# Kernel tuning notes

Hardware: AMD Instinct MI355X
Metric: run time of the kernel (lower is better)

Reference implementation:

```python
import jax, jax.numpy as jnp
import numpy as np

N_HEAD, D_MODEL, D_K, D_V = 8, 512, 64, 64
WINDOW, THRESH = 2, 0.5
TEMP = float(np.sqrt(D_K))
LN_EPS = 1e-5


def setup_inputs() -> dict:
    key = jax.random.key(0)
    ks = jax.random.split(key, 12)
    B, L = 4, 2048
    std_qk = np.sqrt(2.0 / (D_MODEL + D_K))
    std_v = np.sqrt(2.0 / (D_MODEL + D_V))
    return {
        "q": jax.random.normal(ks[0], (B, L, D_MODEL), jnp.float32),
        "k": jax.random.normal(ks[1], (B, L, D_MODEL), jnp.float32),
        "v": jax.random.normal(ks[2], (B, L, D_MODEL), jnp.float32),
        "w_q": jax.random.normal(ks[3], (N_HEAD * D_K, D_MODEL), jnp.float32) * std_qk,
        "b_q": jnp.zeros((N_HEAD * D_K,), jnp.float32),
        "w_k": jax.random.normal(ks[4], (N_HEAD * D_K, D_MODEL), jnp.float32) * std_qk,
        "b_k": jnp.zeros((N_HEAD * D_K,), jnp.float32),
        "w_v": jax.random.normal(ks[5], (N_HEAD * D_V, D_MODEL), jnp.float32) * std_v,
        "b_v": jnp.zeros((N_HEAD * D_V,), jnp.float32),
        "w_g": jax.random.normal(ks[6], (1, D_K), jnp.float32) * (1.0 / np.sqrt(D_K)),
        "b_g": jnp.zeros((1,), jnp.float32),
        "w_fc": jax.random.normal(ks[7], (D_MODEL, N_HEAD * D_V), jnp.float32) * (1.0 / np.sqrt(D_MODEL)),
        "b_fc": jnp.zeros((D_MODEL,), jnp.float32),
        "ln_g": jnp.ones((D_MODEL,), jnp.float32),
        "ln_b": jnp.zeros((D_MODEL,), jnp.float32),
    }


def reference(q, k, v, w_q, b_q, w_k, b_k, w_v, b_v, w_g, b_g, w_fc, b_fc, ln_g, ln_b):
    B, Lq, _ = q.shape
    Lk = k.shape[1]
    residual = q
    # project and split heads: (h, B, L, d)
    qh = (q @ w_q.T + b_q).reshape(B, Lq, N_HEAD, D_K).transpose(2, 0, 1, 3)
    kh = (k @ w_k.T + b_k).reshape(B, Lk, N_HEAD, D_K).transpose(2, 0, 1, 3)
    vh = (v @ w_v.T + b_v).reshape(B, Lk, N_HEAD, D_V).transpose(2, 0, 1, 3)

    scores = jnp.einsum('hbqd,hbkd->hbqk', qh, kh) / TEMP  # (h, B, Lq, Lk)

    # dynamic gate: tokens with sigmoid(gate) > THRESH keep full attention,
    # others are restricted to a +/-WINDOW sliding window
    gate_open = jax.nn.sigmoid(jnp.einsum('hbqd,od->hbqo', qh, w_g) + b_g)[..., 0] > THRESH
    i = jnp.arange(Lq)[:, None]
    j = jnp.arange(Lk)[None, :]
    win = jnp.abs(i - j) <= WINDOW  # (Lq, Lk)
    allowed = gate_open[..., None] | win  # (h, B, Lq, Lk)
    scores = jnp.where(allowed, scores, -jnp.inf)

    attn = jax.nn.softmax(scores, axis=-1)  # dropout is identity in eval
    out = jnp.einsum('hbqk,hbkd->hbqd', attn, vh)
    out = out.transpose(1, 2, 0, 3).reshape(B, Lq, N_HEAD * D_V)
    out = out @ w_fc.T + b_fc

    x = out + residual
    mu = jnp.mean(x, axis=-1, keepdims=True)
    var = jnp.mean((x - mu) ** 2, axis=-1, keepdims=True)
    out = (x - mu) * jax.lax.rsqrt(var + LN_EPS) * ln_g + ln_b

    return out, attn.reshape(N_HEAD * B, Lq, Lk)
```

## Files before the change

kernel.cpp:

```cpp
#include <hip/hip_runtime.h>


typedef _Float16 f16;
typedef _Float16 f16x8 __attribute__((ext_vector_type(8)));
typedef _Float16 f16x4 __attribute__((ext_vector_type(4)));
typedef float f32x4 __attribute__((ext_vector_type(4)));

#define OUT0_ELEMS (4 * 2048 * 512)

__device__ __forceinline__ f16x8 cvt8(float4 a, float4 b) {
  f16x8 r;
  r[0] = (f16)a.x; r[1] = (f16)a.y; r[2] = (f16)a.z; r[3] = (f16)a.w;
  r[4] = (f16)b.x; r[5] = (f16)b.y; r[6] = (f16)b.z; r[7] = (f16)b.w;
  return r;
}

__global__ __launch_bounds__(256) void prep_kernel(
    const float* __restrict__ w_q, const float* __restrict__ b_q,
    const float* __restrict__ w_g, const float* __restrict__ b_g,
    double* __restrict__ wge, double* __restrict__ bqg) {
  int idx = blockIdx.x * 256 + threadIdx.x;
  if (idx < 4096) {
    int h = idx >> 9, c = idx & 511;
    double acc = 0.0;
    for (int d = 0; d < 64; ++d)
      acc += (double)w_g[d] * (double)w_q[(h * 64 + d) * 512 + c];
    wge[idx] = acc;
  }
  if (idx < 8) {
    double acc = (double)b_g[0];
    for (int d = 0; d < 64; ++d)
      acc += (double)b_q[idx * 64 + d] * (double)w_g[d];
    bqg[idx] = acc;
  }
}

__global__ __launch_bounds__(256) void gate_kernel(
    const float* __restrict__ q, const double* __restrict__ wge,
    const double* __restrict__ bqg, int* __restrict__ gate) {
  int lane = threadIdx.x & 63, wid = threadIdx.x >> 6;
  int tok = blockIdx.x * 4 + wid;
  int b = tok >> 11, l = tok & 2047;
  const float* qr = q + (long)tok * 512;
  float qv[8];
#pragma unroll
  for (int j = 0; j < 8; ++j) qv[j] = qr[lane + 64 * j];
#pragma unroll
  for (int h = 0; h < 8; ++h) {
    double acc = 0.0;
#pragma unroll
    for (int j = 0; j < 8; ++j) acc += (double)qv[j] * wge[h * 512 + lane + 64 * j];
#pragma unroll
    for (int off = 1; off < 64; off <<= 1) acc += __shfl_xor(acc, off);
    double logit = acc + bqg[h];
    if (lane == 0) gate[(h * 4 + b) * 2048 + l] = (logit > 0.0) ? 1 : 0;
  }
}

template <int EPI>
__global__ __launch_bounds__(256) void gemm512(
    const float* __restrict__ A, const float* __restrict__ W,
    const float* __restrict__ bias, const float* __restrict__ res,
    f16* __restrict__ out16, float* __restrict__ outf) {
  __shared__ __align__(16) f16 As[64 * 32];
  __shared__ __align__(16) f16 Ws[64 * 32];
  const int tid = threadIdx.x;
  const int lane = tid & 63, wid = tid >> 6;
  const int lo = lane & 15, hi = lane >> 4;
  const int m0 = blockIdx.x * 64, n0 = blockIdx.y * 64;
  const int wm = wid >> 1, wn = wid & 1;

  const int srow = tid >> 2, sseg = tid & 3;
  const int ssu = sseg ^ (srow & 3);
  const float* gA = A + (long)(m0 + srow) * 512 + sseg * 8;
  const float* gW = W + (long)(n0 + srow) * 512 + sseg * 8;
  f16* wA = &As[srow * 32 + ssu * 8];
  f16* wW = &Ws[srow * 32 + ssu * 8];

  const f32x4 zero4 = {0.f, 0.f, 0.f, 0.f};
  f32x4 acc[2][2] = {{zero4, zero4}, {zero4, zero4}};
  const int ra0 = wm * 32 + lo;
  const int rb0 = wn * 32 + lo;
  const int sa = hi ^ (ra0 & 3);
  const int sb = hi ^ (rb0 & 3);

  for (int kk = 0; kk < 512; kk += 32) {
    float4 a0 = *(const float4*)(gA + kk);
    float4 a1 = *(const float4*)(gA + kk + 4);
    float4 w0 = *(const float4*)(gW + kk);
    float4 w1 = *(const float4*)(gW + kk + 4);
    *(f16x8*)wA = cvt8(a0, a1);
    *(f16x8*)wW = cvt8(w0, w1);
    __syncthreads();
    f16x8 af0 = *(const f16x8*)&As[ra0 * 32 + sa * 8];
    f16x8 af1 = *(const f16x8*)&As[(ra0 + 16) * 32 + sa * 8];
    f16x8 bf0 = *(const f16x8*)&Ws[rb0 * 32 + sb * 8];
    f16x8 bf1 = *(const f16x8*)&Ws[(rb0 + 16) * 32 + sb * 8];
    acc[0][0] = __builtin_amdgcn_mfma_f32_16x16x32_f16(af0, bf0, acc[0][0], 0, 0, 0);
    acc[0][1] = __builtin_amdgcn_mfma_f32_16x16x32_f16(af0, bf1, acc[0][1], 0, 0, 0);
    acc[1][0] = __builtin_amdgcn_mfma_f32_16x16x32_f16(af1, bf0, acc[1][0], 0, 0, 0);
    acc[1][1] = __builtin_amdgcn_mfma_f32_16x16x32_f16(af1, bf1, acc[1][1], 0, 0, 0);
    __syncthreads();
  }

#pragma unroll
  for (int i = 0; i < 2; ++i)
#pragma unroll
    for (int j = 0; j < 2; ++j)
#pragma unroll
      for (int r = 0; r < 4; ++r) {
        const int m = m0 + wm * 32 + i * 16 + hi * 4 + r;
        const int n = n0 + wn * 32 + j * 16 + lo;
        float v = acc[i][j][r] + bias[n];
        if constexpr (EPI == 0) {
          const int b = m >> 11, l = m & 2047, h = n >> 6, d = n & 63;
          out16[(long)((h * 4 + b) * 2048 + l) * 64 + d] = (f16)v;
        } else if constexpr (EPI == 2) {
          const int b = m >> 11, l = m & 2047, h = n >> 6, d = n & 63;
          out16[(long)((h * 4 + b) * 64 + d) * 2048 + l] = (f16)v;
        } else {
          outf[(long)m * 512 + n] = v + res[(long)m * 512 + n];
        }
      }
}

struct Stg2 { uint4 d0, d1; };

__device__ __forceinline__ Stg2 ldK(const f16* __restrict__ g, int tid) {
  Stg2 s;
  s.d0 = *(const uint4*)(g + tid * 8);
  s.d1 = *(const uint4*)(g + 2048 + tid * 8);
  return s;
}

__device__ __forceinline__ Stg2 ldV(const f16* __restrict__ g, int tid) {
  const int row = tid >> 3, seg = tid & 7;
  const f16* p = g + (long)row * 2048 + seg * 8;
  Stg2 s;
  s.d0 = *(const uint4*)p;
  s.d1 = *(const uint4*)(p + 32 * 2048);
  return s;
}

__device__ __forceinline__ void stW(const Stg2& s, f16* lds, int tid) {
  const int row = tid >> 3, seg = tid & 7, sw = row & 7;
  *(uint4*)&lds[(row << 6) + ((seg ^ sw) << 3)] = s.d0;
  *(uint4*)&lds[((row + 32) << 6) + ((seg ^ sw) << 3)] = s.d1;
}

__global__ __launch_bounds__(256) void attn_kernel(
    const f16* __restrict__ qh, const f16* __restrict__ kh,
    const f16* __restrict__ vt, const int* __restrict__ gate,
    float* __restrict__ attn, float* __restrict__ o) {
  __shared__ __align__(16) f16 Ks[2][4096];
  __shared__ __align__(16) f16 Vs[2][4096];
  __shared__ __align__(16) f16 Ps[4][1024];
  const int tid = threadIdx.x;
  const int lane = tid & 63, wid = tid >> 6;
  const int lo = lane & 15, hi = lane >> 4;
  const int bid = blockIdx.x;
  const int xcd = bid & 7, local = bid >> 3;
  const int hb = xcd * 4 + (local >> 5);
  const int q0 = (local & 31) << 6;

  const f16* khb = kh + (long)hb * 2048 * 64;
  const f16* vtb = vt + (long)hb * 64 * 2048;

  const f16* qrow = qh + (long)(hb * 2048 + q0 + (wid << 4) + lo) * 64;
  const f16x8 aq0 = *(const f16x8*)(qrow + (hi << 3));
  const f16x8 aq1 = *(const f16x8*)(qrow + 32 + (hi << 3));

  int qi[4], gt[4];
  float psum[4];
#pragma unroll
  for (int r = 0; r < 4; ++r) {
    qi[r] = q0 + (wid << 4) + (hi << 2) + r;
    gt[r] = gate[hb * 2048 + qi[r]];
    psum[r] = 0.f;
  }
  const f32x4 zero4 = {0.f, 0.f, 0.f, 0.f};

  {
    Stg2 kreg = ldK(khb, tid);
    stW(kreg, &Ks[0][0], tid);
    kreg = ldK(khb + 4096, tid);
    int cur = 0;
    for (int kt = 0; kt < 32; ++kt) {
      __syncthreads();
      if (kt < 31) {
        stW(kreg, &Ks[cur ^ 1][0], tid);
        if (kt < 30) kreg = ldK(khb + (long)(kt + 2) * 4096, tid);
      }
      const f16* Kc = &Ks[cur][0];
      f32x4 sacc[4] = {zero4, zero4, zero4, zero4};
      __builtin_amdgcn_s_setprio(1);
#pragma unroll
      for (int s = 0; s < 2; ++s) {
        const f16x8 a = s ? aq1 : aq0;
#pragma unroll
        for (int nt = 0; nt < 4; ++nt) {
          const int krow = (nt << 4) + lo;
          const f16x8 b = *(const f16x8*)&Kc[(krow << 6) + ((((s << 2) + hi) ^ (krow & 7)) << 3)];
          sacc[nt] = __builtin_amdgcn_mfma_f32_16x16x32_f16(a, b, sacc[nt], 0, 0, 0);
        }
      }
      __builtin_amdgcn_s_setprio(0);
      const int kkb = (kt << 6) + lo;
#pragma unroll
      for (int nt = 0; nt < 4; ++nt) {
        const int kk = kkb + (nt << 4);
#pragma unroll
        for (int r = 0; r < 4; ++r) {
          const bool allowed = gt[r] || ((unsigned)(kk - qi[r] + 2) <= 4u);
          psum[r] += allowed ? __expf(sacc[nt][r] * 0.125f) : 0.f;
        }
      }
      cur ^= 1;
    }
  }

  float invl[4];
#pragma unroll
  for (int r = 0; r < 4; ++r) {
    float s = psum[r];
    s += __shfl_xor(s, 1);
    s += __shfl_xor(s, 2);
    s += __shfl_xor(s, 4);
    s += __shfl_xor(s, 8);
    invl[r] = 1.f / s;
  }

  f32x4 oacc[4] = {zero4, zero4, zero4, zero4};
  f16* Pw = &Ps[wid][0];
  const int row2 = lane >> 2, qq = lane & 3;
  float* arow = attn + (long)(hb * 2048 + q0 + (wid << 4) + row2) * 2048;

  {
    Stg2 kreg = ldK(khb, tid);
    Stg2 vreg = ldV(vtb, tid);
    stW(kreg, &Ks[0][0], tid);
    stW(vreg, &Vs[0][0], tid);
    kreg = ldK(khb + 4096, tid);
    vreg = ldV(vtb + 64, tid);
    int cur = 0;
    for (int kt = 0; kt < 32; ++kt) {
      __syncthreads();
      if (kt < 31) {
        stW(kreg, &Ks[cur ^ 1][0], tid);
        stW(vreg, &Vs[cur ^ 1][0], tid);
        if (kt < 30) {
          kreg = ldK(khb + (long)(kt + 2) * 4096, tid);
          vreg = ldV(vtb + ((kt + 2) << 6), tid);
        }
      }
      const f16* Kc = &Ks[cur][0];
      const f16* Vc = &Vs[cur][0];
      f32x4 sacc[4] = {zero4, zero4, zero4, zero4};
      __builtin_amdgcn_s_setprio(1);
#pragma unroll
      for (int s = 0; s < 2; ++s) {
        const f16x8 a = s ? aq1 : aq0;
#pragma unroll
        for (int nt = 0; nt < 4; ++nt) {
          const int krow = (nt << 4) + lo;
          const f16x8 b = *(const f16x8*)&Kc[(krow << 6) + ((((s << 2) + hi) ^ (krow & 7)) << 3)];
          sacc[nt] = __builtin_amdgcn_mfma_f32_16x16x32_f16(a, b, sacc[nt], 0, 0, 0);
        }
      }
      __builtin_amdgcn_s_setprio(0);
      const int kkb = (kt << 6) + lo;
#pragma unroll
      for (int nt = 0; nt < 4; ++nt) {
        const int kk = kkb + (nt << 4);
#pragma unroll
        for (int r = 0; r < 4; ++r) {
          const bool allowed = gt[r] || ((unsigned)(kk - qi[r] + 2) <= 4u);
          const float p = allowed ? __expf(sacc[nt][r] * 0.125f) * invl[r] : 0.f;
          const int prow = (hi << 2) + r;
          const int pcol = (nt << 4) + lo;
          Pw[(prow << 6) + (((pcol >> 3) ^ (prow & 7)) << 3) + (pcol & 7)] = (f16)p;
        }
      }
      __builtin_amdgcn_s_setprio(1);
#pragma unroll
      for (int s = 0; s < 2; ++s) {
        const f16x8 ap = *(const f16x8*)&Pw[(lo << 6) + ((((s << 2) + hi) ^ (lo & 7)) << 3)];
#pragma unroll
        for (int nt = 0; nt < 4; ++nt) {
          const int vrow = (nt << 4) + lo;
          const f16x8 bv = *(const f16x8*)&Vc[(vrow << 6) + ((((s << 2) + hi) ^ (vrow & 7)) << 3)];
          oacc[nt] = __builtin_amdgcn_mfma_f32_16x16x32_f16(ap, bv, oacc[nt], 0, 0, 0);
        }
      }
      __builtin_amdgcn_s_setprio(0);
      {
        const int swz = row2 & 7;
        float* dst = arow + (kt << 6) + (qq << 2);
#pragma unroll
        for (int i = 0; i < 4; ++i) {
          const f16x4 pv = *(const f16x4*)&Pw[(row2 << 6) + ((((i << 1) + (qq >> 1)) ^ swz) << 3) + ((qq & 1) << 2)];
          f32x4 fo = {(float)pv[0], (float)pv[1], (float)pv[2], (float)pv[3]};
          *(f32x4*)(dst + (i << 4)) = fo;
        }
      }
      cur ^= 1;
    }
  }

  const int b = hb & 3, h = hb >> 2;
#pragma unroll
  for (int nt = 0; nt < 4; ++nt)
#pragma unroll
    for (int r = 0; r < 4; ++r)
      o[(long)(b * 2048 + qi[r]) * 512 + (h << 6) + (nt << 4) + lo] = oacc[nt][r];
}

__global__ __launch_bounds__(256) void ln_kernel(float* __restrict__ x,
                                                 const float* __restrict__ g,
                                                 const float* __restrict__ bta) {
  __shared__ float red[8];
  const int t = threadIdx.x;
  float* row = x + (long)blockIdx.x * 512;
  float v0 = row[t], v1 = row[t + 256];
  float s = v0 + v1;
#pragma unroll
  for (int off = 1; off < 64; off <<= 1) s += __shfl_xor(s, off);
  if ((t & 63) == 0) red[t >> 6] = s;
  __syncthreads();
  const float mean = (red[0] + red[1] + red[2] + red[3]) * (1.f / 512.f);
  const float d0 = v0 - mean, d1 = v1 - mean;
  float sq = d0 * d0 + d1 * d1;
#pragma unroll
  for (int off = 1; off < 64; off <<= 1) sq += __shfl_xor(sq, off);
  if ((t & 63) == 0) red[4 + (t >> 6)] = sq;
  __syncthreads();
  const float var = (red[4] + red[5] + red[6] + red[7]) * (1.f / 512.f);
  const float rstd = 1.f / sqrtf(var + 1e-5f);
  row[t] = d0 * rstd * g[t] + bta[t];
  row[t + 256] = d1 * rstd * g[t + 256] + bta[t + 256];
}

extern "C" void kernel_launch(void* const* d_in, const int* in_sizes, int n_in,
                              void* d_out, int out_size, void* d_ws, size_t ws_size,
                              hipStream_t stream) {
  const float* q    = (const float*)d_in[0];
  const float* k    = (const float*)d_in[1];
  const float* v    = (const float*)d_in[2];
  const float* w_q  = (const float*)d_in[3];
  const float* b_q  = (const float*)d_in[4];
  const float* w_k  = (const float*)d_in[5];
  const float* b_k  = (const float*)d_in[6];
  const float* w_v  = (const float*)d_in[7];
  const float* b_v  = (const float*)d_in[8];
  const float* w_g  = (const float*)d_in[9];
  const float* b_g  = (const float*)d_in[10];
  const float* w_fc = (const float*)d_in[11];
  const float* b_fc = (const float*)d_in[12];
  const float* ln_g = (const float*)d_in[13];
  const float* ln_b = (const float*)d_in[14];

  char* wsb = (char*)d_ws;
  f16* qh16   = (f16*)wsb;
  f16* kh16   = qh16 + 4194304;
  f16* vt16   = kh16 + 4194304;
  float* ob   = (float*)(wsb + 25165824);
  int* gateb  = (int*)(wsb + 25165824 + 16777216);
  double* wge = (double*)(wsb + 25165824 + 16777216 + 262144);
  double* bqg = wge + 4096;

  float* out0 = (float*)d_out;
  float* attn = out0 + OUT0_ELEMS;

  prep_kernel<<<16, 256, 0, stream>>>(w_q, b_q, w_g, b_g, wge, bqg);
  gate_kernel<<<2048, 256, 0, stream>>>(q, wge, bqg, gateb);

  dim3 gp(128, 8);
  gemm512<0><<<gp, 256, 0, stream>>>(q, w_q, b_q, nullptr, qh16, nullptr);
  gemm512<0><<<gp, 256, 0, stream>>>(k, w_k, b_k, nullptr, kh16, nullptr);
  gemm512<2><<<gp, 256, 0, stream>>>(v, w_v, b_v, nullptr, vt16, nullptr);

  attn_kernel<<<1024, 256, 0, stream>>>(qh16, kh16, vt16, gateb, attn, ob);

  gemm512<3><<<gp, 256, 0, stream>>>(ob, w_fc, b_fc, q, nullptr, out0);
  ln_kernel<<<8192, 256, 0, stream>>>(out0, ln_g, ln_b);
}
```

Before: 299.4 us.

## Compact gated query rows and handle closed rows with a windowed fast path

Adds a per-head-batch compaction kernel that partitions query rows into gate-open and gate-closed lists. Full dense attention blocks now run only over open rows, addressed through the permutation, and exit early past the open count. Closed rows go to extra blocks that zero the attention row and compute only the 5-wide window softmax and PV product directly. This removes the full QK and PV work for closed rows, at the cost of an extra launch, scattered row addressing, and a serial per-row path for closed rows.

```diff
diff --git a/kernel.cpp b/kernel.cpp
--- a/kernel.cpp
+++ b/kernel.cpp
@@ -55,6 +55,39 @@
     double logit = acc + bqg[h];
     if (lane == 0) gate[(h * 4 + b) * 2048 + l] = (logit > 0.0) ? 1 : 0;
   }
+}
+
+__global__ __launch_bounds__(256) void compact_kernel(
+    const int* __restrict__ gate, unsigned short* __restrict__ perm,
+    int* __restrict__ nopen) {
+  __shared__ int wsum[4];
+  const int hb = blockIdx.x, t = threadIdx.x;
+  const int lane = t & 63, wid = t >> 6;
+  const int base = hb * 2048;
+  int g[8];
+  int cnt = 0;
+#pragma unroll
+  for (int i = 0; i < 8; ++i) { g[i] = gate[base + t * 8 + i]; cnt += g[i]; }
+  int inc = cnt;
+#pragma unroll
+  for (int off = 1; off < 64; off <<= 1) {
+    int y = __shfl_up(inc, off);
+    if (lane >= off) inc += y;
+  }
+  if (lane == 63) wsum[wid] = inc;
+  __syncthreads();
+  int wbase = 0;
+  for (int w = 0; w < wid; ++w) wbase += wsum[w];
+  const int totOpen = wsum[0] + wsum[1] + wsum[2] + wsum[3];
+  int openPos = wbase + inc - cnt;
+  int closedPos = totOpen + t * 8 - openPos;
+#pragma unroll
+  for (int i = 0; i < 8; ++i) {
+    int l = t * 8 + i;
+    if (g[i]) perm[base + openPos++] = (unsigned short)l;
+    else      perm[base + closedPos++] = (unsigned short)l;
+  }
+  if (t == 0) nopen[hb] = totOpen;
 }
 
 template <int EPI>
@@ -151,22 +184,91 @@
 __global__ __launch_bounds__(256) void attn_kernel(
     const f16* __restrict__ qh, const f16* __restrict__ kh,
     const f16* __restrict__ vt, const int* __restrict__ gate,
+    const unsigned short* __restrict__ perm, const int* __restrict__ nopen,
     float* __restrict__ attn, float* __restrict__ o) {
   __shared__ __align__(16) f16 Ks[2][4096];
   __shared__ __align__(16) f16 Vs[2][4096];
   __shared__ __align__(16) f16 Ps[4][1024];
   const int tid = threadIdx.x;
   const int lane = tid & 63, wid = tid >> 6;
+  const int bid = blockIdx.x;
+
+  if (bid >= 1024) {
+    const int vb = bid - 1024;
+    const int hb = vb >> 5, chunk = vb & 31;
+    const int nop = nopen[hb];
+    const int j0 = ((nop + 63) & ~63) + (chunk << 6);
+    if (j0 >= 2048) return;
+    unsigned short* rowIdx = (unsigned short*)&Ks[0][0];
+    if (tid < 64) rowIdx[tid] = perm[hb * 2048 + j0 + tid];
+    __syncthreads();
+    float* abase = attn + ((long)hb * 2048 << 11);
+    const f32x4 zero4 = {0.f, 0.f, 0.f, 0.f};
+#pragma unroll 4
+    for (int it = 0; it < 128; ++it) {
+      const int c = tid + (it << 8);
+      const int ri = c >> 9;
+      const int col = (c & 511) << 2;
+      *(f32x4*)(abase + ((long)rowIdx[ri] << 11) + col) = zero4;
+    }
+    __syncthreads();
+    const f16* qhb = qh + (long)hb * 2048 * 64;
+    const f16* khb = kh + (long)hb * 2048 * 64;
+    const f16* vtb = vt + (long)hb * 64 * 2048;
+    const int b = hb & 3, h = hb >> 2;
+    for (int rr = 0; rr < 16; ++rr) {
+      const int row = rowIdx[(wid << 4) + rr];
+      const int jlo = max(row - 2, 0), jhi = min(row + 2, 2047);
+      const float qv = (float)qhb[(long)row * 64 + lane];
+      float p0, p1, p2, p3, p4, sum = 0.f;
+#pragma unroll
+      for (int jj = 0; jj < 5; ++jj) {
+        const int j = jlo + jj;
+        const int js = min(j, 2047);
+        float prod = qv * (float)khb[(long)js * 64 + lane];
+        prod += __shfl_xor(prod, 1);
+        prod += __shfl_xor(prod, 2);
+        prod += __shfl_xor(prod, 4);
+        prod += __shfl_xor(prod, 8);
+        prod += __shfl_xor(prod, 16);
+        prod += __shfl_xor(prod, 32);
+        const float e = (j <= jhi) ? __expf(prod * 0.125f) : 0.f;
+        if (jj == 0) p0 = e; else if (jj == 1) p1 = e; else if (jj == 2) p2 = e;
+        else if (jj == 3) p3 = e; else p4 = e;
+        sum += e;
+      }
+      const float inv = 1.f / sum;
+      float pv = p0;
+      pv = (lane == 1) ? p1 : pv;
+      pv = (lane == 2) ? p2 : pv;
+      pv = (lane == 3) ? p3 : pv;
+      pv = (lane == 4) ? p4 : pv;
+      if (lane < 5 && (jlo + lane) <= jhi)
+        abase[((long)row << 11) + jlo + lane] = pv * inv;
+      float od = 0.f;
+      od += p0 * (float)vtb[(long)lane * 2048 + min(jlo + 0, 2047)];
+      od += p1 * (float)vtb[(long)lane * 2048 + min(jlo + 1, 2047)];
+      od += p2 * (float)vtb[(long)lane * 2048 + min(jlo + 2, 2047)];
+      od += p3 * (float)vtb[(long)lane * 2048 + min(jlo + 3, 2047)];
+      od += p4 * (float)vtb[(long)lane * 2048 + min(jlo + 4, 2047)];
+      o[(long)(b * 2048 + row) * 512 + (h << 6) + lane] = od * inv;
+    }
+    return;
+  }
+
   const int lo = lane & 15, hi = lane >> 4;
-  const int bid = blockIdx.x;
   const int xcd = bid & 7, local = bid >> 3;
   const int hb = xcd * 4 + (local >> 5);
   const int q0 = (local & 31) << 6;
-
+  const int nop = nopen[hb];
+  if (q0 >= nop) return;
+
+  const unsigned short* pm = perm + hb * 2048 + q0;
   const f16* khb = kh + (long)hb * 2048 * 64;
   const f16* vtb = vt + (long)hb * 64 * 2048;
 
-  const f16* qrow = qh + (long)(hb * 2048 + q0 + (wid << 4) + lo) * 64;
+  const int rowA = pm[(wid << 4) + lo];
+  const f16* qrow = qh + (long)(hb * 2048 + rowA) * 64;
   const f16x8 aq0 = *(const f16x8*)(qrow + (hi << 3));
   const f16x8 aq1 = *(const f16x8*)(qrow + 32 + (hi << 3));
 
@@ -174,7 +276,7 @@
   float psum[4];
 #pragma unroll
   for (int r = 0; r < 4; ++r) {
-    qi[r] = q0 + (wid << 4) + (hi << 2) + r;
+    qi[r] = pm[(wid << 4) + (hi << 2) + r];
     gt[r] = gate[hb * 2048 + qi[r]];
     psum[r] = 0.f;
   }
@@ -233,7 +335,7 @@
   f32x4 oacc[4] = {zero4, zero4, zero4, zero4};
   f16* Pw = &Ps[wid][0];
   const int row2 = lane >> 2, qq = lane & 3;
-  float* arow = attn + (long)(hb * 2048 + q0 + (wid << 4) + row2) * 2048;
+  float* arow = attn + ((long)(hb * 2048 + pm[(wid << 4) + row2]) << 11);
 
   {
     Stg2 kreg = ldK(khb, tid);
@@ -367,19 +469,22 @@
   int* gateb  = (int*)(wsb + 25165824 + 16777216);
   double* wge = (double*)(wsb + 25165824 + 16777216 + 262144);
   double* bqg = wge + 4096;
+  unsigned short* permb = (unsigned short*)(wsb + 25165824 + 16777216 + 262144 + 32768 + 64);
+  int* nopenb = (int*)(wsb + 25165824 + 16777216 + 262144 + 32768 + 64 + 131072);
 
   float* out0 = (float*)d_out;
   float* attn = out0 + OUT0_ELEMS;
 
   prep_kernel<<<16, 256, 0, stream>>>(w_q, b_q, w_g, b_g, wge, bqg);
   gate_kernel<<<2048, 256, 0, stream>>>(q, wge, bqg, gateb);
+  compact_kernel<<<32, 256, 0, stream>>>(gateb, permb, nopenb);
 
   dim3 gp(128, 8);
   gemm512<0><<<gp, 256, 0, stream>>>(q, w_q, b_q, nullptr, qh16, nullptr);
   gemm512<0><<<gp, 256, 0, stream>>>(k, w_k, b_k, nullptr, kh16, nullptr);
   gemm512<2><<<gp, 256, 0, stream>>>(v, w_v, b_v, nullptr, vt16, nullptr);
 
-  attn_kernel<<<1024, 256, 0, stream>>>(qh16, kh16, vt16, gateb, attn, ob);
+  attn_kernel<<<2048, 256, 0, stream>>>(qh16, kh16, vt16, gateb, permb, nopenb, attn, ob);
 
   gemm512<3><<<gp, 256, 0, stream>>>(ob, w_fc, b_fc, q, nullptr, out0);
   ln_kernel<<<8192, 256, 0, stream>>>(out0, ln_g, ln_b);
```

Result: slower. 314.5 us (+5.0%).
